# Performance work log

Measured on AMD Instinct MI355X. Metric: run time of the kernel, lower is better.

The kernel has to match this reference:

```python
import jax, jax.numpy as jnp
import numpy as np
from jax.scipy.ndimage import map_coordinates

ANGLES = 180
PROJ = 180
IMG = 256
THETA_RAD = np.deg2rad(np.linspace(0.0, 180.0, ANGLES, endpoint=False)).astype(np.float32)


def _ramp_filter(size):
    # skimage _get_fourier_filter(size, 'ramp')
    n = np.concatenate((np.arange(1, size // 2 + 1, 2),
                        np.arange(size // 2 - 1, 0, -2)))
    f = np.zeros(size)
    f[0] = 0.25
    f[1::2] = -1.0 / (np.pi * n) ** 2
    return (2.0 * np.real(np.fft.fft(f))).astype(np.float32)


def radon_t(img, theta):
    # skimage radon(circle=True): rotate by each angle (bilinear warp) and sum rows
    N = img.shape[0]
    center = N // 2
    y, x = jnp.mgrid[0:N, 0:N]
    x = x.astype(jnp.float32)
    y = y.astype(jnp.float32)

    def one(th):
        c, s = jnp.cos(th), jnp.sin(th)
        sx = c * x + s * y - center * (c + s - 1.0)   # source col
        sy = -s * x + c * y - center * (c - s - 1.0)  # source row
        rot = map_coordinates(img, [sy, sx], order=1, mode='constant', cval=0.0)
        return rot.sum(axis=0)  # sum over rows -> [N]

    cols = jax.vmap(one)(theta)  # [A, N]
    return cols.T                # [N, A] sinogram


def iradon_t(sino, theta):
    # skimage iradon(circle=True, filter='ramp', interpolation='linear')
    N, A = sino.shape
    pad = max(64, int(2 ** np.ceil(np.log2(2 * N))))
    filt = jnp.asarray(_ramp_filter(pad))
    proj = jnp.fft.fft(jnp.pad(sino, ((0, pad - N), (0, 0))), axis=0) * filt[:, None]
    filtered = jnp.real(jnp.fft.ifft(proj, axis=0)[:N, :]).astype(jnp.float32)  # [N, A]

    radius = N // 2
    xpr, ypr = jnp.mgrid[0:N, 0:N]
    xpr = (xpr - radius).astype(jnp.float32)
    ypr = (ypr - radius).astype(jnp.float32)

    def one(col, th):
        # detector coordinate t, shifted so index 0 corresponds to x[0] = -N//2
        t = ypr * jnp.cos(th) - xpr * jnp.sin(th) + radius
        i0 = jnp.floor(t).astype(jnp.int32)
        frac = t - i0
        v0 = col[jnp.clip(i0, 0, N - 1)]
        v1 = col[jnp.clip(i0 + 1, 0, N - 1)]
        val = (1.0 - frac) * v0 + frac * v1
        inb = (t >= 0.0) & (t <= N - 1.0)  # np.interp(..., left=0, right=0)
        return jnp.where(inb, val, 0.0)

    back = jax.vmap(one)(filtered.T, theta).sum(axis=0)  # [N, N]
    mask = (xpr ** 2 + ypr ** 2) <= radius ** 2
    return jnp.where(mask, back, 0.0) * (jnp.pi / (2.0 * A))


def setup_inputs() -> dict:
    key = jax.random.key(0)
    ks = jax.random.split(key, 7)
    scale = 1.0 / np.sqrt(PROJ)
    return {
        "x": jax.random.normal(ks[0], (4, 3, IMG, IMG), dtype=jnp.float32),
        "Wq": jax.random.normal(ks[1], (PROJ, PROJ), dtype=jnp.float32) * scale,
        "bq": jax.random.normal(ks[2], (PROJ,), dtype=jnp.float32) * scale,
        "Wk": jax.random.normal(ks[3], (PROJ, PROJ), dtype=jnp.float32) * scale,
        "bk": jax.random.normal(ks[4], (PROJ,), dtype=jnp.float32) * scale,
        "Wv": jax.random.normal(ks[5], (PROJ, PROJ), dtype=jnp.float32) * scale,
        "bv": jax.random.normal(ks[6], (PROJ,), dtype=jnp.float32) * scale,
    }


def reference(x, Wq, bq, Wk, bk, Wv, bv):
    B, C, H, W = x.shape
    theta = jnp.asarray(THETA_RAD)
    imgs = x.reshape(B * C, H, W)
    sino = jax.vmap(lambda im: radon_t(im, theta))(imgs)  # [BC, H, A]
    Q = sino @ Wq.T + bq
    K = sino @ Wk.T + bk
    V = sino @ Wv.T + bv
    scores = jax.nn.softmax(
        jnp.einsum('nij,nkj->nik', Q, K) / jnp.sqrt(jnp.float32(PROJ)), axis=-1)
    att = jnp.einsum('nik,nkj->nij', scores, V)            # [BC, H, A]
    rec = jax.vmap(lambda s: iradon_t(s, theta))(att)      # [BC, H, W]
    return rec.reshape(B, C, H, W)
```

## Files before the change

kernel.cpp:

```cpp
#include <hip/hip_runtime.h>

#define AANG 180
#define NN 256
#define BCH 12

#ifndef M_PI
#define M_PI 3.14159265358979323846
#endif

__device__ __forceinline__ int iclamp(int v, int lo, int hi) {
    return v < lo ? lo : (v > hi ? hi : v);
}

#define LSTR 259
#define LROWSMAX 130

__global__ __launch_bounds__(1024, 1)
void radon_kernel(const float* __restrict__ x, float* __restrict__ partial) {
    __shared__ float tile[LROWSMAX * LSTR];
    __shared__ float red[2][1024];
    int blk = blockIdx.x;
    int g = blk % 30;
    int t = blk / 30;
    int h = t & 1;
    int n = t >> 1;
    int tid = threadIdx.x;
    int lx = tid & 255;
    int qid = tid >> 8;
    int R0 = h ? 127 : -1;
    int nrows = h ? 130 : 129;
    float Ylo = h ? 127.0f : -1.0f;
    float Yhi = h ? 255.0f : 126.0f;
    const float* img = x + (size_t)n * NN * NN;

    for (int rr = qid; rr < nrows; rr += 4) {
        int gr = R0 + rr;
        bool rok = (gr >= 0) && (gr < NN);
        const float* row = img + gr * NN;
        int gc = lx - 1;
        tile[rr * LSTR + lx] = (rok && gc >= 0) ? row[gc] : 0.0f;
        if (lx < 3) {
            int gc2 = 255 + lx;
            tile[rr * LSTR + 256 + lx] = (rok && gc2 < NN) ? row[gc2] : 0.0f;
        }
    }
    __syncthreads();

    float fx = (float)lx;
    int ubase = qid * 64;

    for (int pp = 0; pp < 3; ++pp) {
        int a0 = g + (2 * pp) * 30;
        int a1 = a0 + 30;
        float th0 = (float)((double)a0 * (M_PI / 180.0));
        float th1 = (float)((double)a1 * (M_PI / 180.0));
        float c0 = cosf(th0), s0 = sinf(th0);
        float c1 = cosf(th1), s1 = sinf(th1);
        float kx0 = -128.0f * (c0 + s0 - 1.0f), ky0 = -128.0f * (c0 - s0 - 1.0f);
        float kx1 = -128.0f * (c1 + s1 - 1.0f), ky1 = -128.0f * (c1 - s1 - 1.0f);
        float xcon0 = c0 * fx + kx0;
        float dcon0 = -s0 * fx + ky0;
        float xcon1 = c1 * fx + kx1;
        float dcon1 = -s1 * fx + ky1;
        float acc0 = 0.0f, acc1 = 0.0f;
#pragma unroll 2
        for (int i = 0; i < 64; ++i) {
            float fy = (float)(ubase + i);
            float sy0 = __builtin_fmaf(c0, fy, dcon0);
            float sx0 = __builtin_fmaf(s0, fy, xcon0);
            float sy1 = __builtin_fmaf(c1, fy, dcon1);
            float sx1 = __builtin_fmaf(s1, fy, xcon1);
            float iyf0 = floorf(sy0), ixf0 = floorf(sx0);
            float iyf1 = floorf(sy1), ixf1 = floorf(sx1);
            if (iyf0 >= Ylo && iyf0 <= Yhi && ixf0 >= -1.0f && ixf0 <= 255.0f) {
                float wy = sy0 - iyf0, wx = sx0 - ixf0;
                int lr = (int)iyf0 - R0;
                int lc = (int)ixf0 + 1;
                const float* t0 = &tile[lr * LSTR + lc];
                float v00 = t0[0], v01 = t0[1];
                float v10 = t0[LSTR], v11 = t0[LSTR + 1];
                float wx1 = 1.0f - wx, wy1 = 1.0f - wy;
                acc0 += wy1 * (wx1 * v00 + wx * v01) + wy * (wx1 * v10 + wx * v11);
            }
            if (iyf1 >= Ylo && iyf1 <= Yhi && ixf1 >= -1.0f && ixf1 <= 255.0f) {
                float wy = sy1 - iyf1, wx = sx1 - ixf1;
                int lr = (int)iyf1 - R0;
                int lc = (int)ixf1 + 1;
                const float* t1 = &tile[lr * LSTR + lc];
                float v00 = t1[0], v01 = t1[1];
                float v10 = t1[LSTR], v11 = t1[LSTR + 1];
                float wx1 = 1.0f - wx, wy1 = 1.0f - wy;
                acc1 += wy1 * (wx1 * v00 + wx * v01) + wy * (wx1 * v10 + wx * v11);
            }
        }
        if (pp) __syncthreads();
        red[0][tid] = acc0;
        red[1][tid] = acc1;
        __syncthreads();
        if (tid < 256) {
            float r0 = red[0][tid] + red[0][tid + 256] + red[0][tid + 512] + red[0][tid + 768];
            float r1 = red[1][tid] + red[1][tid + 256] + red[1][tid + 512] + red[1][tid + 768];
            size_t base = (((size_t)h * BCH + n) * AANG);
            partial[(base + a0) * NN + tid] = r0;
            partial[(base + a1) * NN + tid] = r1;
        }
    }
}

__global__ void wtrans_kernel(const float* __restrict__ Wq, const float* __restrict__ Wk,
                              const float* __restrict__ Wv, float* __restrict__ WqT,
                              float* __restrict__ WkT, float* __restrict__ WvT) {
    int idx = blockIdx.x * 256 + threadIdx.x;
    if (idx < AANG * AANG) {
        int p = idx / AANG;
        int j = idx - p * AANG;
        int src = j * AANG + p;
        WqT[idx] = Wq[src];
        WkT[idx] = Wk[src];
        WvT[idx] = Wv[src];
    }
}

__global__ void qkv_kernel(const float* __restrict__ partial,
                           const float* __restrict__ WqT, const float* __restrict__ bq,
                           const float* __restrict__ WkT, const float* __restrict__ bk,
                           const float* __restrict__ WvT, const float* __restrict__ bv,
                           float* __restrict__ Q, float* __restrict__ Kt,
                           float* __restrict__ V) {
    __shared__ float srow[8][AANG];
    int blk = blockIdx.x;
    int n = blk >> 5;
    int i0 = (blk & 31) * 8;
    int tid = threadIdx.x;
    const size_t HOFF = (size_t)BCH * AANG * NN;
    if (tid < AANG) {
        for (int r = 0; r < 8; ++r) {
            size_t idx = (((size_t)n) * AANG + tid) * NN + (i0 + r);
            srow[r][tid] = partial[idx] + partial[idx + HOFF];
        }
    }
    __syncthreads();
    if (tid < AANG) {
        int j = tid;
        float aq[8], ak[8], av[8];
        float bqv = bq[j], bkv = bk[j], bvv = bv[j];
        for (int r = 0; r < 8; ++r) { aq[r] = bqv; ak[r] = bkv; av[r] = bvv; }
#pragma unroll 2
        for (int p = 0; p < AANG; ++p) {
            float wq = WqT[p * AANG + j];
            float wk = WkT[p * AANG + j];
            float wv = WvT[p * AANG + j];
#pragma unroll
            for (int r = 0; r < 8; ++r) {
                float sv = srow[r][p];
                aq[r] += sv * wq;
                ak[r] += sv * wk;
                av[r] += sv * wv;
            }
        }
        for (int r = 0; r < 8; ++r) {
            size_t qb = ((size_t)(n * NN + i0 + r)) * AANG + j;
            Q[qb] = aq[r];
            V[qb] = av[r];
        }
        size_t kb = ((size_t)(n * AANG + j)) * NN + i0;
        for (int r = 0; r < 8; ++r) Kt[kb + r] = ak[r];
    }
}

__global__ void attn_kernel(const float* __restrict__ Q, const float* __restrict__ Kt,
                            const float* __restrict__ V, float* __restrict__ att_t) {
    __shared__ float qrow[4][AANG];
    __shared__ float prob[4][NN];
    __shared__ float wm[4][4], wsm[4][4];
    int blk = blockIdx.x;
    int n = blk >> 6;
    int i0 = (blk & 63) * 4;
    int tid = threadIdx.x;
    int wid = tid >> 6;
    if (tid < AANG) {
#pragma unroll
        for (int r = 0; r < 4; ++r)
            qrow[r][tid] = Q[((size_t)(n * NN + i0 + r)) * AANG + tid];
    }
    __syncthreads();
    float d0 = 0.0f, d1 = 0.0f, d2 = 0.0f, d3 = 0.0f;
    const float* kb = Kt + (size_t)n * AANG * NN + tid;
#pragma unroll 4
    for (int j = 0; j < AANG; ++j) {
        float kv = kb[(size_t)j * NN];
        d0 += qrow[0][j] * kv;
        d1 += qrow[1][j] * kv;
        d2 += qrow[2][j] * kv;
        d3 += qrow[3][j] * kv;
    }
    const float rs = 0.0745355992f;
    float l0 = d0 * rs, l1 = d1 * rs, l2 = d2 * rs, l3 = d3 * rs;
    float m0 = l0, m1 = l1, m2 = l2, m3 = l3;
    for (int off = 32; off > 0; off >>= 1) {
        m0 = fmaxf(m0, __shfl_xor(m0, off));
        m1 = fmaxf(m1, __shfl_xor(m1, off));
        m2 = fmaxf(m2, __shfl_xor(m2, off));
        m3 = fmaxf(m3, __shfl_xor(m3, off));
    }
    if ((tid & 63) == 0) { wm[0][wid] = m0; wm[1][wid] = m1; wm[2][wid] = m2; wm[3][wid] = m3; }
    __syncthreads();
    float mx0 = fmaxf(fmaxf(wm[0][0], wm[0][1]), fmaxf(wm[0][2], wm[0][3]));
    float mx1 = fmaxf(fmaxf(wm[1][0], wm[1][1]), fmaxf(wm[1][2], wm[1][3]));
    float mx2 = fmaxf(fmaxf(wm[2][0], wm[2][1]), fmaxf(wm[2][2], wm[2][3]));
    float mx3 = fmaxf(fmaxf(wm[3][0], wm[3][1]), fmaxf(wm[3][2], wm[3][3]));
    float e0 = expf(l0 - mx0), e1 = expf(l1 - mx1);
    float e2 = expf(l2 - mx2), e3 = expf(l3 - mx3);
    float s0 = e0, s1 = e1, s2 = e2, s3 = e3;
    for (int off = 32; off > 0; off >>= 1) {
        s0 += __shfl_xor(s0, off);
        s1 += __shfl_xor(s1, off);
        s2 += __shfl_xor(s2, off);
        s3 += __shfl_xor(s3, off);
    }
    if ((tid & 63) == 0) { wsm[0][wid] = s0; wsm[1][wid] = s1; wsm[2][wid] = s2; wsm[3][wid] = s3; }
    __syncthreads();
    float dn0 = wsm[0][0] + wsm[0][1] + wsm[0][2] + wsm[0][3];
    float dn1 = wsm[1][0] + wsm[1][1] + wsm[1][2] + wsm[1][3];
    float dn2 = wsm[2][0] + wsm[2][1] + wsm[2][2] + wsm[2][3];
    float dn3 = wsm[3][0] + wsm[3][1] + wsm[3][2] + wsm[3][3];
    prob[0][tid] = e0 / dn0;
    prob[1][tid] = e1 / dn1;
    prob[2][tid] = e2 / dn2;
    prob[3][tid] = e3 / dn3;
    __syncthreads();
    if (tid < AANG) {
        float a0 = 0.0f, a1 = 0.0f, a2 = 0.0f, a3 = 0.0f;
        const float* vb = V + (size_t)n * NN * AANG + tid;
#pragma unroll 4
        for (int k = 0; k < NN; ++k) {
            float v = vb[(size_t)k * AANG];
            a0 += prob[0][k] * v;
            a1 += prob[1][k] * v;
            a2 += prob[2][k] * v;
            a3 += prob[3][k] * v;
        }
        float4 st = make_float4(a0, a1, a2, a3);
        *(float4*)&att_t[((size_t)(n * AANG + tid)) * NN + i0] = st;
    }
}

__global__ void filter_kernel(const float* __restrict__ att_t, float* __restrict__ filt) {
    __shared__ float col[NN];
    __shared__ float coef[128];
    int blk = blockIdx.x;
    int tid = threadIdx.x;
    col[tid] = att_t[(size_t)blk * NN + tid];
    if (tid < 128) {
        float d = (float)(2 * tid + 1);
        coef[tid] = -2.0f / ((float)(M_PI * M_PI) * d * d);
    }
    __syncthreads();
    float acc = 0.5f * col[tid];
#pragma unroll 4
    for (int m = 0; m < 128; ++m) {
        int d = 2 * m + 1;
        float lo = (tid - d >= 0) ? col[tid - d] : 0.0f;
        float hi = (tid + d < NN) ? col[tid + d] : 0.0f;
        acc += coef[m] * (lo + hi);
    }
    filt[(size_t)blk * NN + tid] = acc;
}

#define ACH 36
__global__ void backproj_kernel(const float* __restrict__ filt, float* __restrict__ out) {
    __shared__ float cols[ACH][NN];
    __shared__ float cs[AANG], sn[AANG];
    int blk = blockIdx.x;
    int n = blk >> 8;
    int r = blk & 255;
    int tid = threadIdx.x;
    if (tid < AANG) {
        float th = (float)((double)tid * (M_PI / 180.0));
        cs[tid] = cosf(th);
        sn[tid] = sinf(th);
    }
    float xr = (float)(r - 128);
    float yr = (float)(tid - 128);
    float acc = 0.0f;
    const float* fb = filt + (size_t)n * AANG * NN;
    for (int ch = 0; ch < AANG / ACH; ++ch) {
        __syncthreads();
        for (int q = 0; q < ACH; ++q)
            cols[q][tid] = fb[(size_t)(ch * ACH + q) * NN + tid];
        __syncthreads();
#pragma unroll 4
        for (int q = 0; q < ACH; ++q) {
            int aa = ch * ACH + q;
            float t = yr * cs[aa] - xr * sn[aa] + 128.0f;
            float i0f = floorf(t);
            int i0 = (int)i0f;
            float frac = t - i0f;
            int c0 = iclamp(i0, 0, NN - 1);
            int c1 = iclamp(i0 + 1, 0, NN - 1);
            float val = (1.0f - frac) * cols[q][c0] + frac * cols[q][c1];
            if (t >= 0.0f && t <= 255.0f) acc += val;
        }
    }
    bool inside = (xr * xr + yr * yr) <= 16384.0f;
    out[(size_t)blk * NN + tid] = inside ? acc * (float)(M_PI / 360.0) : 0.0f;
}

extern "C" void kernel_launch(void* const* d_in, const int* in_sizes, int n_in,
                              void* d_out, int out_size, void* d_ws, size_t ws_size,
                              hipStream_t stream) {
    const float* x  = (const float*)d_in[0];
    const float* Wq = (const float*)d_in[1];
    const float* bq = (const float*)d_in[2];
    const float* Wk = (const float*)d_in[3];
    const float* bk = (const float*)d_in[4];
    const float* Wv = (const float*)d_in[5];
    const float* bv = (const float*)d_in[6];
    float* out = (float*)d_out;
    float* ws = (float*)d_ws;

    const size_t SZ = (size_t)BCH * NN * AANG;
    float* P     = ws;
    float* Q     = P + 2 * SZ;
    float* Kt    = Q + SZ;
    float* V     = Kt + SZ;
    float* att_t = V + SZ;
    float* WqT   = att_t;
    float* WkT   = WqT + AANG * AANG;
    float* WvT   = WkT + AANG * AANG;
    float* filt  = P;

    wtrans_kernel<<<(AANG * AANG + 255) / 256, 256, 0, stream>>>(Wq, Wk, Wv, WqT, WkT, WvT);
    radon_kernel<<<BCH * 2 * 30, 1024, 0, stream>>>(x, P);
    qkv_kernel<<<BCH * (NN / 8), 256, 0, stream>>>(P, WqT, bq, WkT, bk, WvT, bv, Q, Kt, V);
    attn_kernel<<<BCH * (NN / 4), NN, 0, stream>>>(Q, Kt, V, att_t);
    filter_kernel<<<BCH * AANG, NN, 0, stream>>>(att_t, filt);
    backproj_kernel<<<BCH * NN, NN, 0, stream>>>(filt, out);
}
```

Before: 491.2 us.

## Tighten radon bounds checks, vectorize qkv loads, and batch backprojection rows per block

The radon kernel now uses single unsigned range checks on the integer tile indices and unrolls its inner loop further. The qkv kernel loads the partial sinograms as float4 and stores them transposed in shared memory, so each step reads eight rows with two vector loads. The backprojection kernel now handles four output rows per 1024-thread block, so each staged chunk of filtered columns in shared memory is reused four times and global reloads drop. The trade-off is fewer, larger blocks and more register pressure from the deeper unroll.

```diff
diff --git a/kernel.cpp b/kernel.cpp
--- a/kernel.cpp
+++ b/kernel.cpp
@@ -29,8 +29,7 @@
     int qid = tid >> 8;
     int R0 = h ? 127 : -1;
     int nrows = h ? 130 : 129;
-    float Ylo = h ? 127.0f : -1.0f;
-    float Yhi = h ? 255.0f : 126.0f;
+    unsigned lrmax = h ? 128u : 127u;
     const float* img = x + (size_t)n * NN * NN;
 
     for (int rr = qid; rr < nrows; rr += 4) {
@@ -63,7 +62,7 @@
         float xcon1 = c1 * fx + kx1;
         float dcon1 = -s1 * fx + ky1;
         float acc0 = 0.0f, acc1 = 0.0f;
-#pragma unroll 2
+#pragma unroll 4
         for (int i = 0; i < 64; ++i) {
             float fy = (float)(ubase + i);
             float sy0 = __builtin_fmaf(c0, fy, dcon0);
@@ -72,21 +71,19 @@
             float sx1 = __builtin_fmaf(s1, fy, xcon1);
             float iyf0 = floorf(sy0), ixf0 = floorf(sx0);
             float iyf1 = floorf(sy1), ixf1 = floorf(sx1);
-            if (iyf0 >= Ylo && iyf0 <= Yhi && ixf0 >= -1.0f && ixf0 <= 255.0f) {
+            int lr0 = (int)iyf0 - R0, lc0 = (int)ixf0 + 1;
+            int lr1 = (int)iyf1 - R0, lc1 = (int)ixf1 + 1;
+            if ((unsigned)lr0 <= lrmax && (unsigned)lc0 <= 256u) {
                 float wy = sy0 - iyf0, wx = sx0 - ixf0;
-                int lr = (int)iyf0 - R0;
-                int lc = (int)ixf0 + 1;
-                const float* t0 = &tile[lr * LSTR + lc];
+                const float* t0 = &tile[lr0 * LSTR + lc0];
                 float v00 = t0[0], v01 = t0[1];
                 float v10 = t0[LSTR], v11 = t0[LSTR + 1];
                 float wx1 = 1.0f - wx, wy1 = 1.0f - wy;
                 acc0 += wy1 * (wx1 * v00 + wx * v01) + wy * (wx1 * v10 + wx * v11);
             }
-            if (iyf1 >= Ylo && iyf1 <= Yhi && ixf1 >= -1.0f && ixf1 <= 255.0f) {
+            if ((unsigned)lr1 <= lrmax && (unsigned)lc1 <= 256u) {
                 float wy = sy1 - iyf1, wx = sx1 - ixf1;
-                int lr = (int)iyf1 - R0;
-                int lc = (int)ixf1 + 1;
-                const float* t1 = &tile[lr * LSTR + lc];
+                const float* t1 = &tile[lr1 * LSTR + lc1];
                 float v00 = t1[0], v01 = t1[1];
                 float v10 = t1[LSTR], v11 = t1[LSTR + 1];
                 float wx1 = 1.0f - wx, wy1 = 1.0f - wy;
@@ -127,17 +124,26 @@
                            const float* __restrict__ WvT, const float* __restrict__ bv,
                            float* __restrict__ Q, float* __restrict__ Kt,
                            float* __restrict__ V) {
-    __shared__ float srow[8][AANG];
+    __shared__ float srow_t[AANG][8];
     int blk = blockIdx.x;
     int n = blk >> 5;
     int i0 = (blk & 31) * 8;
     int tid = threadIdx.x;
     const size_t HOFF = (size_t)BCH * AANG * NN;
     if (tid < AANG) {
-        for (int r = 0; r < 8; ++r) {
-            size_t idx = (((size_t)n) * AANG + tid) * NN + (i0 + r);
-            srow[r][tid] = partial[idx] + partial[idx + HOFF];
-        }
+        size_t idx = (((size_t)n) * AANG + tid) * NN + i0;
+        float4 p0 = *(const float4*)&partial[idx];
+        float4 p1 = *(const float4*)&partial[idx + 4];
+        float4 q0 = *(const float4*)&partial[idx + HOFF];
+        float4 q1 = *(const float4*)&partial[idx + HOFF + 4];
+        srow_t[tid][0] = p0.x + q0.x;
+        srow_t[tid][1] = p0.y + q0.y;
+        srow_t[tid][2] = p0.z + q0.z;
+        srow_t[tid][3] = p0.w + q0.w;
+        srow_t[tid][4] = p1.x + q1.x;
+        srow_t[tid][5] = p1.y + q1.y;
+        srow_t[tid][6] = p1.z + q1.z;
+        srow_t[tid][7] = p1.w + q1.w;
     }
     __syncthreads();
     if (tid < AANG) {
@@ -150,13 +156,16 @@
             float wq = WqT[p * AANG + j];
             float wk = WkT[p * AANG + j];
             float wv = WvT[p * AANG + j];
-#pragma unroll
-            for (int r = 0; r < 8; ++r) {
-                float sv = srow[r][p];
-                aq[r] += sv * wq;
-                ak[r] += sv * wk;
-                av[r] += sv * wv;
-            }
+            float4 sv0 = *(const float4*)&srow_t[p][0];
+            float4 sv1 = *(const float4*)&srow_t[p][4];
+            aq[0] += sv0.x * wq; ak[0] += sv0.x * wk; av[0] += sv0.x * wv;
+            aq[1] += sv0.y * wq; ak[1] += sv0.y * wk; av[1] += sv0.y * wv;
+            aq[2] += sv0.z * wq; ak[2] += sv0.z * wk; av[2] += sv0.z * wv;
+            aq[3] += sv0.w * wq; ak[3] += sv0.w * wk; av[3] += sv0.w * wv;
+            aq[4] += sv1.x * wq; ak[4] += sv1.x * wk; av[4] += sv1.x * wv;
+            aq[5] += sv1.y * wq; ak[5] += sv1.y * wk; av[5] += sv1.y * wv;
+            aq[6] += sv1.z * wq; ak[6] += sv1.z * wk; av[6] += sv1.z * wv;
+            aq[7] += sv1.w * wq; ak[7] += sv1.w * wk; av[7] += sv1.w * wv;
         }
         for (int r = 0; r < 8; ++r) {
             size_t qb = ((size_t)(n * NN + i0 + r)) * AANG + j;
@@ -268,26 +277,33 @@
 }
 
 #define ACH 36
-__global__ void backproj_kernel(const float* __restrict__ filt, float* __restrict__ out) {
+__global__ __launch_bounds__(1024)
+void backproj_kernel(const float* __restrict__ filt, float* __restrict__ out) {
     __shared__ float cols[ACH][NN];
     __shared__ float cs[AANG], sn[AANG];
     int blk = blockIdx.x;
-    int n = blk >> 8;
-    int r = blk & 255;
-    int tid = threadIdx.x;
+    int n = blk >> 6;
+    int rg = blk & 63;
+    int tid = threadIdx.x;
+    int col = tid & 255;
+    int rslot = tid >> 8;
+    int r = rg * 4 + rslot;
     if (tid < AANG) {
         float th = (float)((double)tid * (M_PI / 180.0));
         cs[tid] = cosf(th);
         sn[tid] = sinf(th);
     }
     float xr = (float)(r - 128);
-    float yr = (float)(tid - 128);
+    float yr = (float)(col - 128);
     float acc = 0.0f;
     const float* fb = filt + (size_t)n * AANG * NN;
     for (int ch = 0; ch < AANG / ACH; ++ch) {
         __syncthreads();
-        for (int q = 0; q < ACH; ++q)
-            cols[q][tid] = fb[(size_t)(ch * ACH + q) * NN + tid];
+        for (int idx = tid; idx < ACH * NN; idx += 1024) {
+            int q = idx >> 8;
+            int cc = idx & 255;
+            cols[q][cc] = fb[(size_t)(ch * ACH + q) * NN + cc];
+        }
         __syncthreads();
 #pragma unroll 4
         for (int q = 0; q < ACH; ++q) {
@@ -303,7 +319,7 @@
         }
     }
     bool inside = (xr * xr + yr * yr) <= 16384.0f;
-    out[(size_t)blk * NN + tid] = inside ? acc * (float)(M_PI / 360.0) : 0.0f;
+    out[((size_t)(n * NN + r)) * NN + col] = inside ? acc * (float)(M_PI / 360.0) : 0.0f;
 }
 
 extern "C" void kernel_launch(void* const* d_in, const int* in_sizes, int n_in,
@@ -335,5 +351,5 @@
     qkv_kernel<<<BCH * (NN / 8), 256, 0, stream>>>(P, WqT, bq, WkT, bk, WvT, bv, Q, Kt, V);
     attn_kernel<<<BCH * (NN / 4), NN, 0, stream>>>(Q, Kt, V, att_t);
     filter_kernel<<<BCH * AANG, NN, 0, stream>>>(att_t, filt);
-    backproj_kernel<<<BCH * NN, NN, 0, stream>>>(filt, out);
-}
+    backproj_kernel<<<BCH * (NN / 4), 1024, 0, stream>>>(filt, out);
+}
```

New measurement: 463.4 us. -5.7%, faster.
